# Kernel tuning notes

Measured on AMD Instinct MI355X. Metric: run time of the kernel, lower is better.

Reference implementation:

```python
import jax, jax.numpy as jnp
import numpy as np

NUM_TOURS = 200   # fixed segment count (original: tour_index.max()+1)
EPS = 1e-5        # torch InstanceNorm1d default eps


def setup_inputs() -> dict:
    key = jax.random.key(0)
    ks = jax.random.split(key, 9)
    B, P, D = 64, 2000, 128
    embeddings = jax.random.normal(ks[0], (B, P + 1, D), jnp.float32)
    tour_index = jax.random.randint(ks[1], (B, P), 0, NUM_TOURS, dtype=jnp.int32)
    # tour_combiner: Linear(2D -> D); feedforward: Linear(D -> D); stored as (in, out)
    W1 = jax.random.normal(ks[2], (2 * D, D), jnp.float32) / np.sqrt(2 * D)
    b1 = jax.random.normal(ks[3], (D,), jnp.float32) * 0.01
    W2 = jax.random.normal(ks[4], (D, D), jnp.float32) / np.sqrt(D)
    b2 = jax.random.normal(ks[5], (D,), jnp.float32) * 0.01
    # InstanceNorm1d affine params (per channel)
    gamma = 1.0 + 0.1 * jax.random.normal(ks[6], (D,), jnp.float32)
    beta = 0.1 * jax.random.normal(ks[7], (D,), jnp.float32)
    return {
        "batch_size": B, "num_customers": P,
        "tour_index": tour_index, "embeddings": embeddings,
        "W1": W1, "b1": b1, "W2": W2, "b2": b2,
        "gamma": gamma, "beta": beta,
    }


def reference(batch_size, num_customers, tour_index, embeddings, W1, b1, W2, b2, gamma, beta):
    B, P = batch_size, num_customers
    D = embeddings.shape[-1]
    cust = embeddings[:, 1:]                                  # (B, P, D)
    # tour-level segment sum (scatter_add over tour ids, per batch)
    flat_idx = (tour_index + jnp.arange(B, dtype=tour_index.dtype)[:, None] * NUM_TOURS).reshape(-1)
    tour_emb = jax.ops.segment_sum(cust.reshape(B * P, D), flat_idx,
                                   num_segments=B * NUM_TOURS).reshape(B, NUM_TOURS, D)
    # gather tour embedding back to each customer
    cust_tour = jnp.take_along_axis(tour_emb, tour_index[:, :, None], axis=1)  # (B, P, D)
    # concat -> linear -> relu -> linear
    combined = jnp.concatenate([cust, cust_tour], axis=-1)    # (B, P, 2D)
    h = jax.nn.relu(combined @ W1 + b1)
    h = h @ W2 + b2
    # residual + instance norm over the customer axis, per channel
    added = cust + h
    mean = jnp.mean(added, axis=1, keepdims=True)
    var = jnp.var(added, axis=1, keepdims=True)
    normed = (added - mean) * jax.lax.rsqrt(var + EPS) * gamma + beta
    return jnp.concatenate([embeddings[:, :1], normed], axis=1)
```

## Files before the change

### kernel.cpp

```cpp
#include <hip/hip_runtime.h>
#include <stdint.h>

typedef unsigned short u16;
typedef __attribute__((ext_vector_type(8))) short short8;
typedef __attribute__((ext_vector_type(4))) float floatx4;

constexpr int B_ = 64, P_ = 2000, D_ = 128, T_ = 200;

__device__ __forceinline__ u16 f2bf(float f) {
  union { float f; uint32_t u; } v; v.f = f;
  return (u16)((v.u + 0x7fffu + ((v.u >> 16) & 1u)) >> 16);
}
__device__ __forceinline__ float bf2f(u16 u) {
  union { uint32_t u; float f; } v; v.u = ((uint32_t)u) << 16; return v.f;
}

__global__ void k_zero(float* __restrict__ p, int n) {
  int i = blockIdx.x * 256 + threadIdx.x;
  if (i < n) p[i] = 0.f;
}

__global__ void k_prep_w(const float* __restrict__ W1, const float* __restrict__ W2,
                         u16* __restrict__ w1f, u16* __restrict__ w2f) {
  int tid = blockIdx.x * 256 + threadIdx.x;
  if (tid >= 6144) return;
  const float* W = (tid < 4096) ? W1 : W2;
  u16* dst = (tid < 4096) ? w1f : w2f;
  int fid = (tid < 4096) ? tid : tid - 4096;
  int lane = fid & 63;
  int nt = (fid >> 6) & 7;
  int ks = fid >> 9;
  int quad = lane >> 4, c = lane & 15;
  int k0 = ks * 32 + quad * 8;
#pragma unroll
  for (int j = 0; j < 8; ++j)
    dst[(size_t)fid * 8 + j] = f2bf(W[(k0 + j) * D_ + nt * 16 + c]);
}

__global__ __launch_bounds__(256) void k_bin(const int* __restrict__ tidx,
                                             int* __restrict__ list,
                                             int* __restrict__ goff,
                                             int* __restrict__ gcnt) {
  __shared__ int tix[P_];
  __shared__ int cnt[256], scan[256], cur[256];
  const int b = blockIdx.x, tid = threadIdx.x;
  cnt[tid] = 0;
  for (int i = tid; i < P_; i += 256) tix[i] = tidx[b * P_ + i];
  __syncthreads();
  for (int i = tid; i < P_; i += 256) atomicAdd(&cnt[tix[i]], 1);
  __syncthreads();
  scan[tid] = cnt[tid];
  __syncthreads();
  for (int s = 1; s < 256; s <<= 1) {
    int v = (tid >= s) ? scan[tid - s] : 0;
    __syncthreads();
    scan[tid] += v;
    __syncthreads();
  }
  int excl = scan[tid] - cnt[tid];
  if (tid < T_) {
    goff[b * T_ + tid] = excl;
    gcnt[b * T_ + tid] = cnt[tid];
  }
  cur[tid] = excl;
  __syncthreads();
  for (int i = tid; i < P_; i += 256) {
    int slot = atomicAdd(&cur[tix[i]], 1);
    list[b * P_ + slot] = i;
  }
}

__global__ __launch_bounds__(256) void k_gather(const float* __restrict__ emb,
                                                const int* __restrict__ list,
                                                const int* __restrict__ goff,
                                                const int* __restrict__ gcnt,
                                                u16* __restrict__ tourb) {
  const int tid = threadIdx.x;
  const int lane = tid & 63, wv = tid >> 6;
  const int seg = blockIdx.x * 4 + wv;
  const int b = seg / T_;
  const int off = goff[seg], cn = gcnt[seg];
  const int* lstb = list + b * P_;
  const float* eb = emb + ((size_t)(b * 2001 + 1)) * D_ + lane * 2;
  float sx = 0.f, sy = 0.f;
  for (int i = 0; i < cn; i += 8) {
    int pr[8];
#pragma unroll
    for (int j = 0; j < 8; ++j)
      if (i + j < cn) pr[j] = lstb[off + i + j];
    float2 v[8];
#pragma unroll
    for (int j = 0; j < 8; ++j)
      if (i + j < cn) v[j] = *(const float2*)(eb + (size_t)pr[j] * D_);
#pragma unroll
    for (int j = 0; j < 8; ++j)
      if (i + j < cn) { sx += v[j].x; sy += v[j].y; }
  }
  uint32_t pk = (uint32_t)f2bf(sx) | ((uint32_t)f2bf(sy) << 16);
  ((uint32_t*)(tourb + (size_t)seg * D_))[lane] = pk;
}

template <bool BF>
__global__ __launch_bounds__(256) void k_mlp(
    const int* __restrict__ tidx, const float* __restrict__ emb,
    const u16* __restrict__ tourb,
    const u16* __restrict__ w1f, const u16* __restrict__ w2f,
    const float* __restrict__ b1, const float* __restrict__ b2,
    float* __restrict__ ssum, float* __restrict__ ssq,
    u16* __restrict__ addedb, float* __restrict__ out) {
  __shared__ u16 hbuf[128 * 136];
  const int tid = threadIdx.x;
  const int w = tid >> 6, lane = tid & 63, quad = lane >> 4, c = lane & 15;
  const int b = blockIdx.y;
  const int p0 = blockIdx.x * 128;
  const int r0 = w * 32;

  const float* arow[2];
  const u16* trow[2];
#pragma unroll
  for (int mt = 0; mt < 2; ++mt) {
    int p = p0 + r0 + mt * 16 + c;
    int pc = p < P_ ? p : P_ - 1;
    arow[mt] = emb + ((size_t)(b * 2001 + 1 + pc)) * D_;
    int t = tidx[b * P_ + pc];
    trow[mt] = tourb + ((size_t)(b * T_ + t)) * D_;
  }
  float bias1[8], bias2[8];
#pragma unroll
  for (int nt = 0; nt < 8; ++nt) {
    bias1[nt] = b1[nt * 16 + c];
    bias2[nt] = b2[nt * 16 + c];
  }

  floatx4 acc[2][8];
#pragma unroll
  for (int mt = 0; mt < 2; ++mt)
#pragma unroll
    for (int nt = 0; nt < 8; ++nt) acc[mt][nt] = (floatx4)0.f;

#pragma unroll
  for (int ks = 0; ks < 8; ++ks) {
    short8 a[2];
#pragma unroll
    for (int mt = 0; mt < 2; ++mt) {
      if (ks < 4) {
        const float* src = arow[mt] + ks * 32 + quad * 8;
        floatx4 x0 = *(const floatx4*)src;
        floatx4 x1 = *(const floatx4*)(src + 4);
#pragma unroll
        for (int j = 0; j < 4; ++j) {
          a[mt][j]     = (short)f2bf(x0[j]);
          a[mt][4 + j] = (short)f2bf(x1[j]);
        }
      } else {
        a[mt] = *(const short8*)(trow[mt] + (ks - 4) * 32 + quad * 8);
      }
    }
#pragma unroll
    for (int nt = 0; nt < 8; ++nt) {
      short8 bf = *(const short8*)(w1f + ((size_t)((ks * 8 + nt) * 64 + lane)) * 8);
      acc[0][nt] = __builtin_amdgcn_mfma_f32_16x16x32_bf16(a[0], bf, acc[0][nt], 0, 0, 0);
      acc[1][nt] = __builtin_amdgcn_mfma_f32_16x16x32_bf16(a[1], bf, acc[1][nt], 0, 0, 0);
    }
  }

#pragma unroll
  for (int mt = 0; mt < 2; ++mt)
#pragma unroll
    for (int nt = 0; nt < 8; ++nt)
#pragma unroll
      for (int r = 0; r < 4; ++r) {
        int row = r0 + mt * 16 + quad * 4 + r;
        float v = acc[mt][nt][r] + bias1[nt];
        hbuf[row * 136 + nt * 16 + c] = f2bf(v > 0.f ? v : 0.f);
      }
  __syncthreads();

  floatx4 acc2[2][8];
#pragma unroll
  for (int mt = 0; mt < 2; ++mt)
#pragma unroll
    for (int nt = 0; nt < 8; ++nt) acc2[mt][nt] = (floatx4)0.f;

#pragma unroll
  for (int ks = 0; ks < 4; ++ks) {
    short8 a[2];
#pragma unroll
    for (int mt = 0; mt < 2; ++mt)
      a[mt] = *(const short8*)(&hbuf[(r0 + mt * 16 + c) * 136 + ks * 32 + quad * 8]);
#pragma unroll
    for (int nt = 0; nt < 8; ++nt) {
      short8 bf = *(const short8*)(w2f + ((size_t)((ks * 8 + nt) * 64 + lane)) * 8);
      acc2[0][nt] = __builtin_amdgcn_mfma_f32_16x16x32_bf16(a[0], bf, acc2[0][nt], 0, 0, 0);
      acc2[1][nt] = __builtin_amdgcn_mfma_f32_16x16x32_bf16(a[1], bf, acc2[1][nt], 0, 0, 0);
    }
  }

  float cs[8], cq[8];
#pragma unroll
  for (int nt = 0; nt < 8; ++nt) { cs[nt] = 0.f; cq[nt] = 0.f; }
#pragma unroll
  for (int mt = 0; mt < 2; ++mt)
#pragma unroll
    for (int nt = 0; nt < 8; ++nt)
#pragma unroll
      for (int r = 0; r < 4; ++r) {
        int row = r0 + mt * 16 + quad * 4 + r;
        int p = p0 + row;
        int pc = p < P_ ? p : P_ - 1;
        size_t gaddr = ((size_t)(b * 2001 + 1 + pc)) * D_ + nt * 16 + c;
        float add = emb[gaddr] + (acc2[mt][nt][r] + bias2[nt]);
        if (p < P_) {
          if (BF) addedb[((size_t)(b * P_ + p)) * D_ + nt * 16 + c] = f2bf(add);
          else    out[gaddr] = add;
          cs[nt] += add;
          cq[nt] += add * add;
        }
      }
#pragma unroll
  for (int nt = 0; nt < 8; ++nt) {
    cs[nt] += __shfl_xor(cs[nt], 16, 64);
    cs[nt] += __shfl_xor(cs[nt], 32, 64);
    cq[nt] += __shfl_xor(cq[nt], 16, 64);
    cq[nt] += __shfl_xor(cq[nt], 32, 64);
  }
  float* sw = (float*)&hbuf[(size_t)r0 * 136];
  if (quad == 0) {
#pragma unroll
    for (int nt = 0; nt < 8; ++nt) {
      sw[nt * 16 + c] = cs[nt];
      sw[128 + nt * 16 + c] = cq[nt];
    }
  }
  __syncthreads();
  if (tid < 128) {
    float s = 0.f, q = 0.f;
#pragma unroll
    for (int wv = 0; wv < 4; ++wv) {
      const float* sx = (const float*)&hbuf[(size_t)(wv * 32) * 136];
      s += sx[tid];
      q += sx[128 + tid];
    }
    atomicAdd(&ssum[b * D_ + tid], s);
    atomicAdd(&ssq[b * D_ + tid], q);
  }
}

__global__ void k_final(const float* __restrict__ ssum, const float* __restrict__ ssq,
                        const float* __restrict__ gamma, const float* __restrict__ beta,
                        float* __restrict__ scale, float* __restrict__ shift) {
  int i = blockIdx.x * 256 + threadIdx.x;
  if (i >= B_ * D_) return;
  int col = i & 127;
  float mean = ssum[i] * (1.f / P_);
  float var = ssq[i] * (1.f / P_) - mean * mean;
  float rstd = rsqrtf(var + 1e-5f);
  float sc = rstd * gamma[col];
  scale[i] = sc;
  shift[i] = beta[col] - mean * sc;
}

template <bool BF>
__global__ __launch_bounds__(256) void k_out(
    const float* __restrict__ emb, const u16* __restrict__ addedb,
    const float* __restrict__ scale, const float* __restrict__ shift,
    float* __restrict__ out) {
  size_t i = ((size_t)blockIdx.x * 256 + threadIdx.x) * 8;
  int row = (int)(i >> 7), col = (int)(i & 127);
  int b = row / 2001, r = row - b * 2001;
  if (r == 0) {
    *(floatx4*)(out + i)     = *(const floatx4*)(emb + i);
    *(floatx4*)(out + i + 4) = *(const floatx4*)(emb + i + 4);
  } else {
    int cc = b * D_ + col;
    floatx4 a0, a1;
    if (BF) {
      short8 av = *(const short8*)(addedb + ((size_t)(b * P_ + r - 1)) * D_ + col);
#pragma unroll
      for (int j = 0; j < 4; ++j) {
        a0[j] = bf2f((u16)av[j]);
        a1[j] = bf2f((u16)av[4 + j]);
      }
    } else {
      a0 = *(const floatx4*)(out + i);
      a1 = *(const floatx4*)(out + i + 4);
    }
#pragma unroll
    for (int j = 0; j < 4; ++j) {
      a0[j] = a0[j] * scale[cc + j] + shift[cc + j];
      a1[j] = a1[j] * scale[cc + 4 + j] + shift[cc + 4 + j];
    }
    *(floatx4*)(out + i)     = a0;
    *(floatx4*)(out + i + 4) = a1;
  }
}

extern "C" void kernel_launch(void* const* d_in, const int* in_sizes, int n_in,
                              void* d_out, int out_size, void* d_ws, size_t ws_size,
                              hipStream_t stream) {
  const int*   tour_index = (const int*)d_in[2];
  const float* emb   = (const float*)d_in[3];
  const float* W1    = (const float*)d_in[4];
  const float* b1    = (const float*)d_in[5];
  const float* W2    = (const float*)d_in[6];
  const float* b2    = (const float*)d_in[7];
  const float* gamma = (const float*)d_in[8];
  const float* beta  = (const float*)d_in[9];
  float* out = (float*)d_out;
  char* ws = (char*)d_ws;

  u16*   w1f   = (u16*)(ws);
  u16*   w2f   = (u16*)(ws + 65536);
  float* ssum  = (float*)(ws + 98304);
  float* ssq   = ssum + B_ * D_;
  float* scale = (float*)(ws + 163840);
  float* shift = scale + B_ * D_;
  u16*   tourb = (u16*)(ws + 229376);
  int*   list  = (int*)(ws + 3506176);
  int*   goff  = (int*)(ws + 4018176);
  int*   gcnt  = (int*)(ws + 4069376);
  u16*   addedb = (u16*)(ws + 4120576);
  const bool big = ws_size >= (size_t)4120576 + 32768000;

  hipLaunchKernelGGL(k_zero,   dim3(64),     dim3(256), 0, stream, ssum, 2 * B_ * D_);
  hipLaunchKernelGGL(k_prep_w, dim3(24),     dim3(256), 0, stream, W1, W2, w1f, w2f);
  hipLaunchKernelGGL(k_bin,    dim3(64),     dim3(256), 0, stream, tour_index, list, goff, gcnt);
  hipLaunchKernelGGL(k_gather, dim3(3200),   dim3(256), 0, stream, emb, list, goff, gcnt, tourb);
  if (big) {
    hipLaunchKernelGGL(HIP_KERNEL_NAME(k_mlp<true>), dim3(16, 64), dim3(256), 0, stream,
                       tour_index, emb, tourb, w1f, w2f, b1, b2, ssum, ssq, addedb, out);
  } else {
    hipLaunchKernelGGL(HIP_KERNEL_NAME(k_mlp<false>), dim3(16, 64), dim3(256), 0, stream,
                       tour_index, emb, tourb, w1f, w2f, b1, b2, ssum, ssq, addedb, out);
  }
  hipLaunchKernelGGL(k_final,  dim3(32),     dim3(256), 0, stream, ssum, ssq, gamma, beta,
                     scale, shift);
  if (big) {
    hipLaunchKernelGGL(HIP_KERNEL_NAME(k_out<true>),  dim3(8004), dim3(256), 0, stream,
                       emb, addedb, scale, shift, out);
  } else {
    hipLaunchKernelGGL(HIP_KERNEL_NAME(k_out<false>), dim3(8004), dim3(256), 0, stream,
                       emb, addedb, scale, shift, out);
  }
}
```

Baseline: 225.5 us.

## Merge setup kernels, fold stat finalize into output kernel, stage bf16 stores via LDS

Combines the zeroing, weight-repacking and binning kernels into one multi-role setup launch, and removes the separate finalize kernel by having each output block compute scale/shift for its batch(es) into shared memory. In the MLP kernel, the bf16 residual values are first written to LDS and then copied out as coalesced 16-byte rows instead of scattered 2-byte global stores. This cuts launch count and uncoalesced writes, at the cost of an extra barrier and redundant per-block statistics math.

```diff
diff --git a/kernel.cpp b/kernel.cpp
--- a/kernel.cpp
+++ b/kernel.cpp
@@ -15,58 +15,55 @@
   union { uint32_t u; float f; } v; v.u = ((uint32_t)u) << 16; return v.f;
 }
 
-__global__ void k_zero(float* __restrict__ p, int n) {
-  int i = blockIdx.x * 256 + threadIdx.x;
-  if (i < n) p[i] = 0.f;
-}
-
-__global__ void k_prep_w(const float* __restrict__ W1, const float* __restrict__ W2,
-                         u16* __restrict__ w1f, u16* __restrict__ w2f) {
-  int tid = blockIdx.x * 256 + threadIdx.x;
-  if (tid >= 6144) return;
-  const float* W = (tid < 4096) ? W1 : W2;
-  u16* dst = (tid < 4096) ? w1f : w2f;
-  int fid = (tid < 4096) ? tid : tid - 4096;
-  int lane = fid & 63;
-  int nt = (fid >> 6) & 7;
-  int ks = fid >> 9;
-  int quad = lane >> 4, c = lane & 15;
-  int k0 = ks * 32 + quad * 8;
-#pragma unroll
-  for (int j = 0; j < 8; ++j)
-    dst[(size_t)fid * 8 + j] = f2bf(W[(k0 + j) * D_ + nt * 16 + c]);
-}
-
-__global__ __launch_bounds__(256) void k_bin(const int* __restrict__ tidx,
-                                             int* __restrict__ list,
-                                             int* __restrict__ goff,
-                                             int* __restrict__ gcnt) {
+__global__ __launch_bounds__(256) void k_setup(
+    const int* __restrict__ tidx, const float* __restrict__ W1,
+    const float* __restrict__ W2, u16* __restrict__ w1f, u16* __restrict__ w2f,
+    int* __restrict__ list, int* __restrict__ goff, int* __restrict__ gcnt,
+    float* __restrict__ ssum) {
   __shared__ int tix[P_];
   __shared__ int cnt[256], scan[256], cur[256];
-  const int b = blockIdx.x, tid = threadIdx.x;
-  cnt[tid] = 0;
-  for (int i = tid; i < P_; i += 256) tix[i] = tidx[b * P_ + i];
-  __syncthreads();
-  for (int i = tid; i < P_; i += 256) atomicAdd(&cnt[tix[i]], 1);
-  __syncthreads();
-  scan[tid] = cnt[tid];
-  __syncthreads();
-  for (int s = 1; s < 256; s <<= 1) {
-    int v = (tid >= s) ? scan[tid - s] : 0;
+  const int bid = blockIdx.x, tid = threadIdx.x;
+  if (bid < 64) {
+    const int b = bid;
+    cnt[tid] = 0;
+    for (int i = tid; i < P_; i += 256) tix[i] = tidx[b * P_ + i];
     __syncthreads();
-    scan[tid] += v;
+    for (int i = tid; i < P_; i += 256) atomicAdd(&cnt[tix[i]], 1);
     __syncthreads();
-  }
-  int excl = scan[tid] - cnt[tid];
-  if (tid < T_) {
-    goff[b * T_ + tid] = excl;
-    gcnt[b * T_ + tid] = cnt[tid];
-  }
-  cur[tid] = excl;
-  __syncthreads();
-  for (int i = tid; i < P_; i += 256) {
-    int slot = atomicAdd(&cur[tix[i]], 1);
-    list[b * P_ + slot] = i;
+    scan[tid] = cnt[tid];
+    __syncthreads();
+    for (int s = 1; s < 256; s <<= 1) {
+      int v = (tid >= s) ? scan[tid - s] : 0;
+      __syncthreads();
+      scan[tid] += v;
+      __syncthreads();
+    }
+    int excl = scan[tid] - cnt[tid];
+    if (tid < T_) {
+      goff[b * T_ + tid] = excl;
+      gcnt[b * T_ + tid] = cnt[tid];
+    }
+    cur[tid] = excl;
+    __syncthreads();
+    for (int i = tid; i < P_; i += 256) {
+      int slot = atomicAdd(&cur[tix[i]], 1);
+      list[b * P_ + slot] = i;
+    }
+  } else if (bid < 88) {
+    int t = (bid - 64) * 256 + tid;
+    const float* W = (t < 4096) ? W1 : W2;
+    u16* dst = (t < 4096) ? w1f : w2f;
+    int fid = (t < 4096) ? t : t - 4096;
+    int lane = fid & 63;
+    int nt = (fid >> 6) & 7;
+    int ks = fid >> 9;
+    int quad = lane >> 4, c = lane & 15;
+    int k0 = ks * 32 + quad * 8;
+#pragma unroll
+    for (int j = 0; j < 8; ++j)
+      dst[(size_t)fid * 8 + j] = f2bf(W[(k0 + j) * D_ + nt * 16 + c]);
+  } else {
+    ssum[(bid - 88) * 256 + tid] = 0.f;
   }
 }
 
@@ -109,6 +106,7 @@
     float* __restrict__ ssum, float* __restrict__ ssq,
     u16* __restrict__ addedb, float* __restrict__ out) {
   __shared__ u16 hbuf[128 * 136];
+  __shared__ float sstat[4][256];
   const int tid = threadIdx.x;
   const int w = tid >> 6, lane = tid & 63, quad = lane >> 4, c = lane & 15;
   const int b = blockIdx.y;
@@ -195,6 +193,7 @@
       acc2[1][nt] = __builtin_amdgcn_mfma_f32_16x16x32_bf16(a[1], bf, acc2[1][nt], 0, 0, 0);
     }
   }
+  __syncthreads();
 
   float cs[8], cq[8];
 #pragma unroll
@@ -211,11 +210,11 @@
         size_t gaddr = ((size_t)(b * 2001 + 1 + pc)) * D_ + nt * 16 + c;
         float add = emb[gaddr] + (acc2[mt][nt][r] + bias2[nt]);
         if (p < P_) {
-          if (BF) addedb[((size_t)(b * P_ + p)) * D_ + nt * 16 + c] = f2bf(add);
-          else    out[gaddr] = add;
           cs[nt] += add;
           cq[nt] += add * add;
+          if (!BF) out[gaddr] = add;
         }
+        if (BF) hbuf[row * 136 + nt * 16 + c] = f2bf(add);
       }
 #pragma unroll
   for (int nt = 0; nt < 8; ++nt) {
@@ -224,55 +223,69 @@
     cq[nt] += __shfl_xor(cq[nt], 16, 64);
     cq[nt] += __shfl_xor(cq[nt], 32, 64);
   }
-  float* sw = (float*)&hbuf[(size_t)r0 * 136];
   if (quad == 0) {
 #pragma unroll
     for (int nt = 0; nt < 8; ++nt) {
-      sw[nt * 16 + c] = cs[nt];
-      sw[128 + nt * 16 + c] = cq[nt];
+      sstat[w][nt * 16 + c] = cs[nt];
+      sstat[w][128 + nt * 16 + c] = cq[nt];
     }
   }
   __syncthreads();
+
+  if (BF) {
+#pragma unroll
+    for (int it = 0; it < 8; ++it) {
+      int idx = it * 256 + tid;
+      int row = idx >> 4, col = (idx & 15) * 8;
+      int p = p0 + row;
+      if (p < P_) {
+        short8 hv = *(const short8*)&hbuf[row * 136 + col];
+        *(short8*)(addedb + ((size_t)(b * P_ + p)) * D_ + col) = hv;
+      }
+    }
+  }
   if (tid < 128) {
     float s = 0.f, q = 0.f;
 #pragma unroll
     for (int wv = 0; wv < 4; ++wv) {
-      const float* sx = (const float*)&hbuf[(size_t)(wv * 32) * 136];
-      s += sx[tid];
-      q += sx[128 + tid];
+      s += sstat[wv][tid];
+      q += sstat[wv][128 + tid];
     }
     atomicAdd(&ssum[b * D_ + tid], s);
     atomicAdd(&ssq[b * D_ + tid], q);
   }
-}
-
-__global__ void k_final(const float* __restrict__ ssum, const float* __restrict__ ssq,
-                        const float* __restrict__ gamma, const float* __restrict__ beta,
-                        float* __restrict__ scale, float* __restrict__ shift) {
-  int i = blockIdx.x * 256 + threadIdx.x;
-  if (i >= B_ * D_) return;
-  int col = i & 127;
-  float mean = ssum[i] * (1.f / P_);
-  float var = ssq[i] * (1.f / P_) - mean * mean;
-  float rstd = rsqrtf(var + 1e-5f);
-  float sc = rstd * gamma[col];
-  scale[i] = sc;
-  shift[i] = beta[col] - mean * sc;
 }
 
 template <bool BF>
 __global__ __launch_bounds__(256) void k_out(
     const float* __restrict__ emb, const u16* __restrict__ addedb,
-    const float* __restrict__ scale, const float* __restrict__ shift,
+    const float* __restrict__ ssum, const float* __restrict__ ssq,
+    const float* __restrict__ gamma, const float* __restrict__ beta,
     float* __restrict__ out) {
-  size_t i = ((size_t)blockIdx.x * 256 + threadIdx.x) * 8;
+  __shared__ float sc[2][128], sh[2][128];
+  const int tid = threadIdx.x;
+  const int row0 = blockIdx.x * 16;
+  const int b0 = row0 / 2001;
+  const int b1 = (row0 + 15) / 2001;
+  {
+    int which = tid >> 7, col = tid & 127;
+    int bb = which ? b1 : b0;
+    float mean = ssum[bb * D_ + col] * (1.f / P_);
+    float var = ssq[bb * D_ + col] * (1.f / P_) - mean * mean;
+    float rstd = rsqrtf(var + 1e-5f);
+    float scv = rstd * gamma[col];
+    sc[which][col] = scv;
+    sh[which][col] = beta[col] - mean * scv;
+  }
+  __syncthreads();
+  size_t i = (size_t)blockIdx.x * 2048 + (size_t)tid * 8;
   int row = (int)(i >> 7), col = (int)(i & 127);
   int b = row / 2001, r = row - b * 2001;
   if (r == 0) {
     *(floatx4*)(out + i)     = *(const floatx4*)(emb + i);
     *(floatx4*)(out + i + 4) = *(const floatx4*)(emb + i + 4);
   } else {
-    int cc = b * D_ + col;
+    const int wb = (b == b0) ? 0 : 1;
     floatx4 a0, a1;
     if (BF) {
       short8 av = *(const short8*)(addedb + ((size_t)(b * P_ + r - 1)) * D_ + col);
@@ -287,8 +300,8 @@
     }
 #pragma unroll
     for (int j = 0; j < 4; ++j) {
-      a0[j] = a0[j] * scale[cc + j] + shift[cc + j];
-      a1[j] = a1[j] * scale[cc + 4 + j] + shift[cc + 4 + j];
+      a0[j] = a0[j] * sc[wb][col + j] + sh[wb][col + j];
+      a1[j] = a1[j] * sc[wb][col + 4 + j] + sh[wb][col + 4 + j];
     }
     *(floatx4*)(out + i)     = a0;
     *(floatx4*)(out + i + 4) = a1;
@@ -313,33 +326,26 @@
   u16*   w2f   = (u16*)(ws + 65536);
   float* ssum  = (float*)(ws + 98304);
   float* ssq   = ssum + B_ * D_;
-  float* scale = (float*)(ws + 163840);
-  float* shift = scale + B_ * D_;
-  u16*   tourb = (u16*)(ws + 229376);
-  int*   list  = (int*)(ws + 3506176);
-  int*   goff  = (int*)(ws + 4018176);
-  int*   gcnt  = (int*)(ws + 4069376);
-  u16*   addedb = (u16*)(ws + 4120576);
-  const bool big = ws_size >= (size_t)4120576 + 32768000;
-
-  hipLaunchKernelGGL(k_zero,   dim3(64),     dim3(256), 0, stream, ssum, 2 * B_ * D_);
-  hipLaunchKernelGGL(k_prep_w, dim3(24),     dim3(256), 0, stream, W1, W2, w1f, w2f);
-  hipLaunchKernelGGL(k_bin,    dim3(64),     dim3(256), 0, stream, tour_index, list, goff, gcnt);
-  hipLaunchKernelGGL(k_gather, dim3(3200),   dim3(256), 0, stream, emb, list, goff, gcnt, tourb);
+  u16*   tourb = (u16*)(ws + 163840);
+  int*   list  = (int*)(ws + 3440640);
+  int*   goff  = (int*)(ws + 3952640);
+  int*   gcnt  = (int*)(ws + 4003840);
+  u16*   addedb = (u16*)(ws + 4055040);
+  const bool big = ws_size >= (size_t)4055040 + 32768000;
+
+  hipLaunchKernelGGL(k_setup,  dim3(152),  dim3(256), 0, stream,
+                     tour_index, W1, W2, w1f, w2f, list, goff, gcnt, ssum);
+  hipLaunchKernelGGL(k_gather, dim3(3200), dim3(256), 0, stream,
+                     emb, list, goff, gcnt, tourb);
   if (big) {
     hipLaunchKernelGGL(HIP_KERNEL_NAME(k_mlp<true>), dim3(16, 64), dim3(256), 0, stream,
                        tour_index, emb, tourb, w1f, w2f, b1, b2, ssum, ssq, addedb, out);
+    hipLaunchKernelGGL(HIP_KERNEL_NAME(k_out<true>), dim3(8004), dim3(256), 0, stream,
+                       emb, addedb, ssum, ssq, gamma, beta, out);
   } else {
     hipLaunchKernelGGL(HIP_KERNEL_NAME(k_mlp<false>), dim3(16, 64), dim3(256), 0, stream,
                        tour_index, emb, tourb, w1f, w2f, b1, b2, ssum, ssq, addedb, out);
-  }
-  hipLaunchKernelGGL(k_final,  dim3(32),     dim3(256), 0, stream, ssum, ssq, gamma, beta,
-                     scale, shift);
-  if (big) {
-    hipLaunchKernelGGL(HIP_KERNEL_NAME(k_out<true>),  dim3(8004), dim3(256), 0, stream,
-                       emb, addedb, scale, shift, out);
-  } else {
     hipLaunchKernelGGL(HIP_KERNEL_NAME(k_out<false>), dim3(8004), dim3(256), 0, stream,
-                       emb, addedb, scale, shift, out);
-  }
-}
+                       emb, addedb, ssum, ssq, gamma, beta, out);
+  }
+}
```

New measurement: 237.5 us. +5.3%, slower.
